# Optimization experiments

Hardware: AMD Instinct MI355X
Metric: run time of the kernel (lower is better)

## Reference

```python
import jax, jax.numpy as jnp
import numpy as np

T = 32  # simulation_length
L = 4   # number of NeuralCores in the chain


def to_uniform_spikes(x, cycle, sim_len):
    """Uniform spike encoding: emit round(x*T) spikes evenly spaced over T cycles.
    Faithful to SpikingUnifiedCoreFlow.to_uniform_spikes."""
    N = jnp.round(x * sim_len).astype(jnp.int32)
    mask = (N != 0) & (N != sim_len) & (cycle < sim_len)
    N_safe = jnp.maximum(N, 1)
    spacing = sim_len / N_safe.astype(x.dtype)          # T / N
    fire = mask & (jnp.floor(cycle / spacing) < N_safe) & (jnp.floor(jnp.mod(cycle, spacing)) == 0)
    out = fire.astype(x.dtype)
    return jnp.where(N == sim_len, jnp.ones_like(out), out)  # saturated channels fire every cycle


def setup_inputs() -> dict:
    key = jax.random.key(0)
    k0, k1 = jax.random.split(key)
    x = jax.random.uniform(k0, (128, 1024), dtype=jnp.float32)          # activations in [0,1]
    weights = jax.random.normal(k1, (L, 1024, 1024), dtype=jnp.float32) * 0.02  # (neurons, axons) per core
    thresholds = jnp.ones((L,), dtype=jnp.float32)
    return {"x": x, "weights": weights, "thresholds": thresholds}


def reference(x, weights, thresholds):
    """Rate-mode spiking simulation over a chain of NeuralCores.
    Per cycle: encode input to spikes (Uniform), propagate through cores with
    LIF integration (membrane += W @ spikes; spike = threshold < membrane;
    membrane -= spike * threshold), output = mean spike train of last core."""
    B = x.shape[0]
    H = weights.shape[1]

    def step(mem, cycle):
        sig = to_uniform_spikes(x, cycle, T)            # (B, axons_in)
        new_mems = []
        for l in range(L):
            m = mem[l] + sig @ weights[l].T             # F.linear(sig, W)
            s = (thresholds[l] < m).astype(x.dtype)     # thresholding_mode '<'
            m = m - s * thresholds[l]                   # Default firing: subtract reset
            new_mems.append(m)
            sig = s                                     # feed downstream core this cycle
        return jnp.stack(new_mems), sig                 # sig = last core spikes

    mem0 = jnp.zeros((L, B, H), dtype=x.dtype)
    _, out_spikes = jax.lax.scan(step, mem0, jnp.arange(T))  # (T, B, H)
    return out_spikes.mean(axis=0)                      # spike counts -> rates
```

## Files before the change

### kernel.cpp

```cpp
#include <hip/hip_runtime.h>
#include <stdint.h>


typedef __attribute__((ext_vector_type(4)))  int   i32x4;
typedef __attribute__((ext_vector_type(16))) int   i32x16;
typedef __attribute__((ext_vector_type(4)))  float f32x4;

#define SCALE_F 4294967296.0f
#define NSL 4

__device__ __forceinline__ void gload16(const void* g, void* l) {
    __builtin_amdgcn_global_load_lds(
        (const __attribute__((address_space(1))) void*)g,
        (__attribute__((address_space(3))) void*)l, 16, 0, 0);
}

__device__ __forceinline__ i32x4 expand16(unsigned int f) {
    i32x4 r;
    #pragma unroll
    for (int d = 0; d < 4; ++d)
        r[d] = (int)((((f >> (4 * d)) & 0xFu) * 0x00204081u) & 0x01010101u);
    return r;
}

__device__ __forceinline__ void digits4(const float* __restrict__ w,
                                        signed char* __restrict__ planes,
                                        int layer, int rest4) {
    f32x4 wv = *reinterpret_cast<const f32x4*>(w + ((size_t)layer << 20) + rest4);
    long long q[4];
    #pragma unroll
    for (int i = 0; i < 4; ++i) q[i] = llrintf(wv[i] * SCALE_F);
    #pragma unroll
    for (int s = 0; s < NSL; ++s) {
        uint32_t pack = 0;
        #pragma unroll
        for (int i = 0; i < 4; ++i) {
            int d = (int)(signed char)((unsigned char)(q[i] & 255));
            q[i] = (q[i] - d) >> 8;
            pack |= ((uint32_t)(unsigned char)d) << (8 * i);
        }
        *reinterpret_cast<uint32_t*>(planes + (((size_t)(layer * NSL + s)) << 20) + rest4) = pack;
    }
}

__global__ void k_prep(const float* __restrict__ x, const float* __restrict__ w,
                       uint32_t* __restrict__ Am, signed char* __restrict__ planes) {
    if (blockIdx.x < 1024) {
        int tid = blockIdx.x * 256 + threadIdx.x;
        digits4(w, planes, 0, tid << 2);
    } else {
        const int wid  = ((blockIdx.x - 1024) * 256 + threadIdx.x) >> 6;
        const int lane = threadIdx.x & 63;
        const int b = wid >> 4, kc = wid & 15;
        float v = x[b * 1024 + kc * 64 + lane];
        int N = (int)rintf(v * 32.0f);
        uint32_t bits = 0;
        if (N >= 32) {
            bits = 0xFFFFFFFFu;
        } else if (N > 0) {
            float spacing = 32.0f / (float)N;
            #pragma unroll
            for (int t = 0; t < 32; ++t) {
                float fm = fmodf((float)t, spacing);
                if (fm < 1.0f) bits |= (1u << t);
            }
        }
        uint32_t cap = 0;
        #pragma unroll
        for (int t = 0; t < 32; ++t) {
            unsigned long long bal = __ballot((bits >> t) & 1u);
            if (lane == t)      cap = (uint32_t)bal;
            if (lane == t + 32) cap = (uint32_t)(bal >> 32);
        }
        const int t = lane & 31, ww = lane >> 5;
        Am[(size_t)(b * 32 + t) * 32 + kc * 2 + ww] = cap;
    }
}

__global__ __launch_bounds__(512, 4) void k_fused(
        const uint32_t* __restrict__ Am,
        signed char* __restrict__ planes,
        const float* __restrict__ th,
        const float* __restrict__ w,
        uint32_t* __restrict__ AmNext,
        float* __restrict__ out,
        int layer, int dlayer) {
    __shared__ alignas(16) signed char lds[2][32768];

    const int tid  = threadIdx.x;
    const int lane = tid & 63;
    const int wave = tid >> 6;
    const int mw   = wave >> 1;
    const int nw   = wave & 1;
    const int lr   = lane & 31;
    const int hi   = lane >> 5;

    const int xc = blockIdx.x & 7, q = blockIdx.x >> 3;
    const int nTile = xc * 2 + (q & 1);
    const int mTile = q >> 1;
    const int mBase = mTile * 128, nBase = nTile * 64;

    const signed char* srcB[NSL];
    {
        const int r0 = tid >> 3, qs = tid & 7;
        const int sw0 = (qs ^ (r0 & 7)) * 16;
        #pragma unroll
        for (int s = 0; s < NSL; ++s)
            srcB[s] = planes + (((size_t)(layer * NSL + s)) << 20)
                    + (size_t)(nBase + r0) * 1024 + sw0;
    }
    const uint32_t* aRow = Am + (size_t)(mBase + mw * 32 + lr) * 32;

    int baddr[4];
    {
        const int brow = nw * 32 + lr;
        #pragma unroll
        for (int ks = 0; ks < 4; ++ks)
            baddr[ks] = brow * 128 + (((ks * 2 + hi) ^ (brow & 7)) * 16);
    }

    i32x16 acc[NSL];
    #pragma unroll
    for (int s = 0; s < NSL; ++s)
        #pragma unroll
        for (int r = 0; r < 16; ++r) acc[s][r] = 0;

    auto STAGE = [&](int buf, int c) {
        const int ko = c * 128;
        gload16(srcB[0] + ko, &lds[buf][0]     + tid * 16);
        gload16(srcB[1] + ko, &lds[buf][8192]  + tid * 16);
        gload16(srcB[2] + ko, &lds[buf][16384] + tid * 16);
        gload16(srcB[3] + ko, &lds[buf][24576] + tid * 16);
    };

    i32x4 amr[2];
    STAGE(0, 0);
    amr[0] = *reinterpret_cast<const i32x4*>(aRow);

    #pragma unroll
    for (int c = 0; c < 8; ++c) {
        const int buf = c & 1;
        const signed char* lb = &lds[buf][0];

        asm volatile("s_waitcnt vmcnt(0)" ::: "memory");
        __builtin_amdgcn_s_barrier();
        asm volatile("" ::: "memory");

        if (c + 1 < 8) {
            STAGE(buf ^ 1, c + 1);
            amr[(c + 1) & 1] = *reinterpret_cast<const i32x4*>(aRow + (c + 1) * 4);
        }

        i32x4 af[4];
        #pragma unroll
        for (int ks = 0; ks < 4; ++ks)
            af[ks] = expand16((((unsigned)amr[c & 1][ks]) >> (16 * hi)) & 0xFFFFu);

        __builtin_amdgcn_s_setprio(1);
        #pragma unroll
        for (int ks = 0; ks < 4; ++ks) {
            #pragma unroll
            for (int s = 0; s < NSL; ++s) {
                i32x4 bf = *reinterpret_cast<const i32x4*>(lb + s * 8192 + baddr[ks]);
                acc[s] = __builtin_amdgcn_mfma_i32_32x32x32_i8(af[ks], bf, acc[s], 0, 0, 0);
            }
        }
        __builtin_amdgcn_s_setprio(0);
    }

    const long long TH = llrintf(th[layer] * SCALE_F);
    const int batch = mTile * 4 + mw;
    uint32_t bits = 0;
    long long mmem = 0;
    #pragma unroll
    for (int half = 0; half < 2; ++half) {
        long long own[8], par[8];
        #pragma unroll
        for (int r = 0; r < 8; ++r) {
            long long v = 0;
            #pragma unroll
            for (int s = 0; s < NSL; ++s)
                v += ((long long)acc[s][half * 8 + r]) << (8 * s);
            own[r] = v;
        }
        #pragma unroll
        for (int r = 0; r < 8; ++r) {
            int plo = __shfl((int)(uint32_t)own[r], lane ^ 32, 64);
            int phi = __shfl((int)(own[r] >> 32), lane ^ 32, 64);
            par[r] = ((long long)phi << 32) | (uint32_t)plo;
        }
        #pragma unroll
        for (int tq = 0; tq < 16; ++tq) {
            const int idx = (tq >> 3) * 4 + (tq & 3);
            const int usePar = ((tq >> 2) & 1) ^ hi;
            long long v = usePar ? par[idx] : own[idx];
            mmem += v;
            if (mmem > TH) { mmem -= TH; bits |= (1u << (half * 16 + tq)); }
        }
    }

    if (AmNext) {
        uint32_t cap = 0;
        #pragma unroll
        for (int t = 0; t < 32; ++t) {
            unsigned long long bal = __ballot((bits >> t) & 1u);
            if (lane == t) cap = (uint32_t)bal;
        }
        if (hi == 0)
            AmNext[(size_t)(batch * 32 + lr) * 32 + nTile * 2 + nw] = cap;
    } else if (hi == 0) {
        out[batch * 1024 + nBase + nw * 32 + lr] = (float)__popc(bits) * 0.03125f;
    }

    if (dlayer < 4)
        digits4(w, planes, dlayer, (blockIdx.x * 512 + tid) << 2);
}

extern "C" void kernel_launch(void* const* d_in, const int* in_sizes, int n_in,
                              void* d_out, int out_size, void* d_ws, size_t ws_size,
                              hipStream_t stream) {
    const float* x  = (const float*)d_in[0];
    const float* w  = (const float*)d_in[1];
    const float* th = (const float*)d_in[2];
    float* out = (float*)d_out;
    char* ws = (char*)d_ws;

    signed char* planes = (signed char*)(ws);
    uint32_t*    Am0    = (uint32_t*)(ws + 16777216);
    uint32_t*    Am1    = (uint32_t*)(ws + 17301504);

    k_prep<<<1536, 256, 0, stream>>>(x, w, Am0, planes);

    uint32_t* Ain = Am0;
    uint32_t* Anx = Am1;
    for (int l = 0; l < 4; ++l) {
        k_fused<<<512, 512, 0, stream>>>(Ain, planes, th, w,
                                         (l < 3) ? Anx : nullptr,
                                         (l == 3) ? out : nullptr,
                                         l, l + 1);
        uint32_t* tmp = Ain; Ain = Anx; Anx = tmp;
    }
}
```

Baseline: 104.0 us.

## Store weight digit planes in MFMA fragment order and load directly to registers

The int8 digit planes are now written in a fragment-major layout that matches the MFMA B-operand, so each lane loads its 16-byte fragments straight from global memory into registers. This removes the LDS staging, the per-chunk barriers and the swizzled LDS reads. A three-bank register pipeline prefetches two half-chunks ahead. Launch bounds drop from 4 to 2 blocks per CU to leave room for the extra registers. In exchange there is no shared-memory reuse across waves, so each wave fetches its own B data from global or L2, and occupancy may be lower.

```diff
diff --git a/kernel.cpp b/kernel.cpp
--- a/kernel.cpp
+++ b/kernel.cpp
@@ -9,12 +9,6 @@
 #define SCALE_F 4294967296.0f
 #define NSL 4
 
-__device__ __forceinline__ void gload16(const void* g, void* l) {
-    __builtin_amdgcn_global_load_lds(
-        (const __attribute__((address_space(1))) void*)g,
-        (__attribute__((address_space(3))) void*)l, 16, 0, 0);
-}
-
 __device__ __forceinline__ i32x4 expand16(unsigned int f) {
     i32x4 r;
     #pragma unroll
@@ -23,31 +17,43 @@
     return r;
 }
 
-__device__ __forceinline__ void digits4(const float* __restrict__ w,
-                                        signed char* __restrict__ planes,
-                                        int layer, int rest4) {
-    f32x4 wv = *reinterpret_cast<const f32x4*>(w + ((size_t)layer << 20) + rest4);
-    long long q[4];
-    #pragma unroll
-    for (int i = 0; i < 4; ++i) q[i] = llrintf(wv[i] * SCALE_F);
+__device__ __forceinline__ void digits_frag(const float* __restrict__ w,
+                                            signed char* __restrict__ planes,
+                                            int layer, int gtid) {
+    const int b2 = gtid & 3;
+    const int hi = (gtid >> 2) & 1;
+    const int rw = (gtid >> 3) & 31;
+    const int rq = (gtid >> 8) & 1;
+    const int ks = (gtid >> 9) & 3;
+    const int c  = (gtid >> 11) & 7;
+    const int nT = gtid >> 14;
+    const int n  = nT * 64 + rq * 32 + rw;
+    const int k  = c * 128 + ks * 32 + hi * 16 + b2 * 4;
+    f32x4 wv = *reinterpret_cast<const f32x4*>(
+            w + ((size_t)layer << 20) + (size_t)n * 1024 + k);
+    long long qv[4];
+    #pragma unroll
+    for (int i = 0; i < 4; ++i) qv[i] = llrintf(wv[i] * SCALE_F);
+    const size_t base = ((size_t)layer << 22) + ((size_t)nT << 18)
+                      + (size_t)c * 32768 + ks * 2048 + rq * 1024
+                      + rw * 32 + hi * 16 + b2 * 4;
     #pragma unroll
     for (int s = 0; s < NSL; ++s) {
         uint32_t pack = 0;
         #pragma unroll
         for (int i = 0; i < 4; ++i) {
-            int d = (int)(signed char)((unsigned char)(q[i] & 255));
-            q[i] = (q[i] - d) >> 8;
+            int d = (int)(signed char)((unsigned char)(qv[i] & 255));
+            qv[i] = (qv[i] - d) >> 8;
             pack |= ((uint32_t)(unsigned char)d) << (8 * i);
         }
-        *reinterpret_cast<uint32_t*>(planes + (((size_t)(layer * NSL + s)) << 20) + rest4) = pack;
+        *reinterpret_cast<uint32_t*>(planes + base + (size_t)s * 8192) = pack;
     }
 }
 
 __global__ void k_prep(const float* __restrict__ x, const float* __restrict__ w,
                        uint32_t* __restrict__ Am, signed char* __restrict__ planes) {
     if (blockIdx.x < 1024) {
-        int tid = blockIdx.x * 256 + threadIdx.x;
-        digits4(w, planes, 0, tid << 2);
+        digits_frag(w, planes, 0, blockIdx.x * 256 + threadIdx.x);
     } else {
         const int wid  = ((blockIdx.x - 1024) * 256 + threadIdx.x) >> 6;
         const int lane = threadIdx.x & 63;
@@ -77,7 +83,7 @@
     }
 }
 
-__global__ __launch_bounds__(512, 4) void k_fused(
+__global__ __launch_bounds__(512, 2) void k_fused(
         const uint32_t* __restrict__ Am,
         signed char* __restrict__ planes,
         const float* __restrict__ th,
@@ -85,8 +91,6 @@
         uint32_t* __restrict__ AmNext,
         float* __restrict__ out,
         int layer, int dlayer) {
-    __shared__ alignas(16) signed char lds[2][32768];
-
     const int tid  = threadIdx.x;
     const int lane = tid & 63;
     const int wave = tid >> 6;
@@ -100,70 +104,57 @@
     const int mTile = q >> 1;
     const int mBase = mTile * 128, nBase = nTile * 64;
 
-    const signed char* srcB[NSL];
+    const signed char* fb[NSL][2];
     {
-        const int r0 = tid >> 3, qs = tid & 7;
-        const int sw0 = (qs ^ (r0 & 7)) * 16;
+        const signed char* pb = planes + ((size_t)layer << 22)
+                              + ((size_t)nTile << 18)
+                              + nw * 1024 + lr * 32 + hi * 16;
         #pragma unroll
         for (int s = 0; s < NSL; ++s)
-            srcB[s] = planes + (((size_t)(layer * NSL + s)) << 20)
-                    + (size_t)(nBase + r0) * 1024 + sw0;
+            #pragma unroll
+            for (int h = 0; h < 2; ++h)
+                fb[s][h] = pb + s * 8192 + h * 4096;
     }
     const uint32_t* aRow = Am + (size_t)(mBase + mw * 32 + lr) * 32;
 
-    int baddr[4];
-    {
-        const int brow = nw * 32 + lr;
-        #pragma unroll
-        for (int ks = 0; ks < 4; ++ks)
-            baddr[ks] = brow * 128 + (((ks * 2 + hi) ^ (brow & 7)) * 16);
-    }
-
     i32x16 acc[NSL];
     #pragma unroll
     for (int s = 0; s < NSL; ++s)
         #pragma unroll
         for (int r = 0; r < 16; ++r) acc[s][r] = 0;
 
-    auto STAGE = [&](int buf, int c) {
-        const int ko = c * 128;
-        gload16(srcB[0] + ko, &lds[buf][0]     + tid * 16);
-        gload16(srcB[1] + ko, &lds[buf][8192]  + tid * 16);
-        gload16(srcB[2] + ko, &lds[buf][16384] + tid * 16);
-        gload16(srcB[3] + ko, &lds[buf][24576] + tid * 16);
+    i32x4 B[3][2][NSL];
+    i32x4 amr[2];
+
+    auto LOADG = [&](int bank, int c, int h) {
+        #pragma unroll
+        for (int kp = 0; kp < 2; ++kp)
+            #pragma unroll
+            for (int s = 0; s < NSL; ++s)
+                B[bank][kp][s] = *reinterpret_cast<const i32x4*>(
+                        fb[s][h] + (size_t)c * 32768 + kp * 2048);
     };
 
-    i32x4 amr[2];
-    STAGE(0, 0);
+    LOADG(0, 0, 0);
     amr[0] = *reinterpret_cast<const i32x4*>(aRow);
-
-    #pragma unroll
-    for (int c = 0; c < 8; ++c) {
-        const int buf = c & 1;
-        const signed char* lb = &lds[buf][0];
-
-        asm volatile("s_waitcnt vmcnt(0)" ::: "memory");
-        __builtin_amdgcn_s_barrier();
-        asm volatile("" ::: "memory");
-
-        if (c + 1 < 8) {
-            STAGE(buf ^ 1, c + 1);
+    LOADG(1, 0, 1);
+
+    #pragma unroll
+    for (int g = 0; g < 16; ++g) {
+        const int c = g >> 1, h = g & 1, bank = g % 3;
+        if (g + 2 < 16) LOADG((g + 2) % 3, (g + 2) >> 1, (g + 2) & 1);
+        if (h == 0 && c + 1 < 8)
             amr[(c + 1) & 1] = *reinterpret_cast<const i32x4*>(aRow + (c + 1) * 4);
-        }
-
-        i32x4 af[4];
-        #pragma unroll
-        for (int ks = 0; ks < 4; ++ks)
-            af[ks] = expand16((((unsigned)amr[c & 1][ks]) >> (16 * hi)) & 0xFFFFu);
 
         __builtin_amdgcn_s_setprio(1);
         #pragma unroll
-        for (int ks = 0; ks < 4; ++ks) {
-            #pragma unroll
-            for (int s = 0; s < NSL; ++s) {
-                i32x4 bf = *reinterpret_cast<const i32x4*>(lb + s * 8192 + baddr[ks]);
-                acc[s] = __builtin_amdgcn_mfma_i32_32x32x32_i8(af[ks], bf, acc[s], 0, 0, 0);
-            }
+        for (int kp = 0; kp < 2; ++kp) {
+            i32x4 af = expand16(
+                (((unsigned)amr[c & 1][h * 2 + kp]) >> (16 * hi)) & 0xFFFFu);
+            #pragma unroll
+            for (int s = 0; s < NSL; ++s)
+                acc[s] = __builtin_amdgcn_mfma_i32_32x32x32_i8(
+                        af, B[bank][kp][s], acc[s], 0, 0, 0);
         }
         __builtin_amdgcn_s_setprio(0);
     }
@@ -213,7 +204,7 @@
     }
 
     if (dlayer < 4)
-        digits4(w, planes, dlayer, (blockIdx.x * 512 + tid) << 2);
+        digits_frag(w, planes, dlayer, blockIdx.x * 512 + tid);
 }
 
 extern "C" void kernel_launch(void* const* d_in, const int* in_sizes, int n_in,
```

Measured after the change: 125.5 us. 20.7% more time.
